# Optimization experiments

Measured on AMD Instinct MI355X. Metric: run time of the kernel, lower is better.

## Reference

```python
import jax, jax.numpy as jnp
import numpy as np

STRIDE, K, PAD = 2, 4, 1
DN = ('NCH', 'OIH', 'NCH')


def conv1d(x, w, b):
    # w: (out, in, k); stride-2, pad-1 conv matching nn.Conv1d(k=4,s=2,p=1)
    y = jax.lax.conv_general_dilated(x, w, (STRIDE,), ((PAD, PAD),), dimension_numbers=DN)
    return y + b[None, :, None]


def conv_transpose1d(x, w, b):
    # w: (in, out, k) torch ConvTranspose1d layout. Equivalent forward conv:
    # dilate input by stride, pad k-1-p=2 each side, flipped+transposed kernel.
    wf = jnp.flip(w, -1).transpose(1, 0, 2)  # (out, in, k)
    y = jax.lax.conv_general_dilated(x, wf, (1,), ((K - 1 - PAD, K - 1 - PAD),),
                                     lhs_dilation=(STRIDE,), dimension_numbers=DN)
    return y + b[None, :, None]


def setup_inputs() -> dict:
    key = jax.random.key(0)
    ks = jax.random.split(key, 9)
    s = 0.1  # keep activations stable through 6 layers
    return {
        'x': jax.random.normal(ks[0], (16, 1, 65536), dtype=jnp.float32),
        'enc_w0': jax.random.normal(ks[1], (64, 1, 4), dtype=jnp.float32) * s,
        'enc_w': jax.random.normal(ks[2], (5, 64, 64, 4), dtype=jnp.float32) * s,
        'enc_b': jax.random.normal(ks[3], (6, 64), dtype=jnp.float32) * s,
        'codebook': jax.random.normal(ks[4], (1024, 64), dtype=jnp.float32),
        'dec_w': jax.random.normal(ks[5], (5, 64, 64, 4), dtype=jnp.float32) * s,
        'dec_w_last': jax.random.normal(ks[6], (64, 1, 4), dtype=jnp.float32) * s,
        'dec_b': jax.random.normal(ks[7], (5, 64), dtype=jnp.float32) * s,
        'dec_b_last': jax.random.normal(ks[8], (1,), dtype=jnp.float32) * s,
    }


def reference(x, enc_w0, enc_w, enc_b, codebook, dec_w, dec_w_last, dec_b, dec_b_last):
    B = x.shape[0]
    D = codebook.shape[1]

    h = jax.nn.relu(conv1d(x, enc_w0, enc_b[0]))
    for i in range(5):
        h = jax.nn.relu(conv1d(h, enc_w[i], enc_b[i + 1]))
    # h: (B, D, L'); flatten tokens
    z_e = h.transpose(0, 2, 1).reshape(-1, D)  # (B*L', D)

    # ---- Vector quantize: squared-distance argmin + gather ----
    dist = (jnp.sum(z_e * z_e, axis=1, keepdims=True)
            - 2.0 * z_e @ codebook.T
            + jnp.sum(codebook * codebook, axis=1)[None, :])  # (B*L', C)
    ids = jnp.argmin(dist, axis=-1)
    e = codebook[ids]
    e_k = z_e + jax.lax.stop_gradient(e - z_e)  # straight-through

    g = e_k.reshape(B, -1, D).transpose(0, 2, 1)  # (B, D, L')

    for i in range(5):
        g = jax.nn.relu(conv_transpose1d(g, dec_w[i], dec_b[i]))
    y = conv_transpose1d(g, dec_w_last, dec_b_last)
    return y, z_e, ids
```

## Files before the change

kernel.cpp:

```cpp
#include <hip/hip_runtime.h>

#define CH 64

typedef short s16x8 __attribute__((ext_vector_type(8)));
typedef float f32x4 __attribute__((ext_vector_type(4)));

static __device__ __forceinline__ ushort f2bf(float f) {
    union { float f; uint u; } v; v.f = f;
    const uint r = (v.u + 0x7FFFu + ((v.u >> 16) & 1u)) >> 16;
    return (ushort)r;
}
static __device__ __forceinline__ float bf2f(ushort u) {
    union { uint u; float f; } v; v.u = ((uint)u) << 16; return v.f;
}

__global__ __launch_bounds__(256) void k_prepack_enc(
    const float* __restrict__ enc_w, float* __restrict__ encW)
{
    const int idx = blockIdx.x * 256 + threadIdx.x;
    const int tau = idx & 3;
    const int o = (idx >> 2) & 63;
    const int i = (idx >> 8) & 63;
    const int L = idx >> 14;
    encW[idx] = enc_w[(((size_t)L * 64 + o) * 64 + i) * 4 + tau];
}

#define ACC4(A, W, L, H) \
    A = fmaf((W).w, (H).y, fmaf((W).z, (H).x, fmaf((W).y, (L).y, fmaf((W).x, (L).x, (A)))))

template<int T>
__device__ __forceinline__ void conv_accum_t(
    const float (*inT)[2 * T + 8], const float* __restrict__ wpk, int ibase,
    float acc[4][T / 16], int og, int pg)
{
    const float* wI = wpk + og * 16 + (size_t)ibase * 256;
    for (int ii = 0; ii < 16; ++ii) {
        const float* wp = wI + ii * 256;
        const float4 w0 = *(const float4*)(wp + 0);
        const float4 w1 = *(const float4*)(wp + 4);
        const float4 w2 = *(const float4*)(wp + 8);
        const float4 w3 = *(const float4*)(wp + 12);
        const float* row = inT[ii];
#pragma unroll
        for (int j = 0; j < T / 32; ++j) {
            const int base = 4 * pg + 64 * j;
            const float2 xa = *(const float2*)(row + base);
            const float2 xb = *(const float2*)(row + base + 2);
            const float2 xc = *(const float2*)(row + base + 4);
            ACC4(acc[0][2*j],   w0, xa, xb);
            ACC4(acc[1][2*j],   w1, xa, xb);
            ACC4(acc[2][2*j],   w2, xa, xb);
            ACC4(acc[3][2*j],   w3, xa, xb);
            ACC4(acc[0][2*j+1], w0, xb, xc);
            ACC4(acc[1][2*j+1], w1, xb, xc);
            ACC4(acc[2][2*j+1], w2, xb, xc);
            ACC4(acc[3][2*j+1], w3, xb, xc);
        }
    }
}

template<int T>
__device__ __forceinline__ void conv_epilogue_t(
    float acc[4][T / 16], float* __restrict__ out,
    int b, int m0, int Lout, int transpose, int og, int pg)
{
    if (!transpose) {
#pragma unroll
        for (int oo = 0; oo < 4; ++oo) {
            float* ob = out + ((size_t)b * CH + og * 4 + oo) * Lout + m0 + 2 * pg;
#pragma unroll
            for (int j = 0; j < T / 32; ++j) {
                float2 v;
                v.x = fmaxf(acc[oo][2*j], 0.f);
                v.y = fmaxf(acc[oo][2*j+1], 0.f);
                *(float2*)(ob + 32 * j) = v;
            }
        }
    } else {
#pragma unroll
        for (int j = 0; j < T / 32; ++j)
#pragma unroll
            for (int h = 0; h < 2; ++h) {
                const int ml = 2 * pg + 32 * j + h;
                float* ob = out + ((size_t)b * Lout + m0 + ml) * CH + og * 4;
                float4 v;
                v.x = fmaxf(acc[0][2*j+h], 0.f);
                v.y = fmaxf(acc[1][2*j+h], 0.f);
                v.z = fmaxf(acc[2][2*j+h], 0.f);
                v.w = fmaxf(acc[3][2*j+h], 0.f);
                *(float4*)ob = v;
            }
    }
}

template<int T>
__global__ __launch_bounds__(256) void k_enc_conv_t(
    const float* __restrict__ in, const float* __restrict__ wpk,
    const float* __restrict__ bias, float* __restrict__ out,
    int Lin, int Lout, int transpose)
{
    __shared__ float inT[16][2 * T + 8];
    const int m0 = blockIdx.x * T;
    const int b = blockIdx.y;
    const int tid = threadIdx.x;
    const int og = tid >> 4, pg = tid & 15;
    const float* inb = in + (size_t)b * CH * Lin;
    float acc[4][T / 16];
#pragma unroll
    for (int oo = 0; oo < 4; ++oo) {
        const float bv = bias[og * 4 + oo];
#pragma unroll
        for (int j = 0; j < T / 16; ++j) acc[oo][j] = bv;
    }
    for (int q = 0; q < 4; ++q) {
        {
            const int r = tid >> 4;
            const int i = q * 16 + r;
            const int seg = tid & 15;
            const float* src = inb + (size_t)i * Lin + 2 * m0 + (T / 8) * seg;
            float* dst = inT[r] + 1 + (T / 8) * seg;
#pragma unroll
            for (int t = 0; t < T / 32; ++t) {
                const float4 v = *(const float4*)(src + 4 * t);
                float* d = dst + 4 * t;
                d[0] = v.x;
                *(float2*)(d + 1) = make_float2(v.y, v.z);
                d[3] = v.w;
            }
            if (tid < 32) {
                const int rr = tid & 15, side = tid >> 4;
                const int pl = side ? (2 * T + 1) : 0;
                const int p = 2 * m0 - 1 + pl;
                inT[rr][pl] = (p >= 0 && p < Lin) ? inb[(size_t)(q * 16 + rr) * Lin + p] : 0.f;
            }
        }
        __syncthreads();
        conv_accum_t<T>(inT, wpk, q * 16, acc, og, pg);
        __syncthreads();
    }
    conv_epilogue_t<T>(acc, out, b, m0, Lout, transpose, og, pg);
}

__global__ __launch_bounds__(256) void k_enc01(
    const float* __restrict__ x, const float* __restrict__ w0,
    const float* __restrict__ b0, const float* __restrict__ wpk0,
    const float* __restrict__ b1, float* __restrict__ out)
{
    __shared__ float xl[520];
    __shared__ float e0s[16][264];
    const int m0 = blockIdx.x * 128;
    const int b = blockIdx.y;
    const int tid = threadIdx.x;
    const int og = tid >> 4, pg = tid & 15;
    const bool interior = (blockIdx.x != 0) && (blockIdx.x != gridDim.x - 1);
    const float* xb = x + (size_t)b * 65536;
    const int x0i = 4 * m0 - 3;
    if (interior) {
        for (int xi = tid; xi < 518; xi += 256) xl[xi] = xb[x0i + xi];
    } else {
        for (int xi = tid; xi < 518; xi += 256) {
            const int q = x0i + xi;
            xl[xi] = (q >= 0 && q < 65536) ? xb[q] : 0.f;
        }
    }
    float acc[4][8];
#pragma unroll
    for (int oo = 0; oo < 4; ++oo) {
        const float bv = b1[og * 4 + oo];
#pragma unroll
        for (int j = 0; j < 8; ++j) acc[oo][j] = bv;
    }
    const int r = tid >> 4;
    const int oct = tid & 15;
    const int pbase = 2 * m0 - 1;
    __syncthreads();
    for (int q = 0; q < 4; ++q) {
        {
            const int i = q * 16 + r;
            const float4 wv = *(const float4*)(w0 + i * 4);
            const float bv = b0[i];
            if (interior) {
                for (int t = 0; t < 17; ++t) {
                    const int pl = oct * 17 + t;
                    if (pl < 258) {
                        const float* xp = xl + 2 * pl;
                        const float v = fmaf(wv.w, xp[3], fmaf(wv.z, xp[2],
                                        fmaf(wv.y, xp[1], fmaf(wv.x, xp[0], bv))));
                        e0s[r][pl] = fmaxf(v, 0.f);
                    }
                }
            } else {
                for (int t = 0; t < 17; ++t) {
                    const int pl = oct * 17 + t;
                    if (pl < 258) {
                        const int pe = pbase + pl;
                        const float* xp = xl + 2 * pl;
                        const float v = fmaf(wv.w, xp[3], fmaf(wv.z, xp[2],
                                        fmaf(wv.y, xp[1], fmaf(wv.x, xp[0], bv))));
                        e0s[r][pl] = (pe >= 0 && pe < 32768) ? fmaxf(v, 0.f) : 0.f;
                    }
                }
            }
        }
        __syncthreads();
        conv_accum_t<128>(e0s, wpk0, q * 16, acc, og, pg);
        __syncthreads();
    }
    conv_epilogue_t<128>(acc, out, b, m0, 16384, 0, og, pg);
}

__global__ __launch_bounds__(512) void k_vq(
    const float* __restrict__ z, const float* __restrict__ cb,
    float* __restrict__ idsf, ushort* __restrict__ g)
{
    __shared__ float c2s[1024];
    __shared__ float rval[8][64];
    __shared__ int   ridx[8][64];
    __shared__ int   widx[64];
    const int t0 = blockIdx.x * 64;
    const int tid = threadIdx.x;
    const int lane = tid & 63;
    const int wv = __builtin_amdgcn_readfirstlane(tid >> 6);

    for (int c = tid; c < 1024; c += 512) {
        const float* cp = cb + (size_t)c * 64;
        float s0 = 0.f, s1 = 0.f, s2 = 0.f, s3 = 0.f;
#pragma unroll
        for (int d = 0; d < 64; d += 4) {
            const float4 v = *(const float4*)(cp + d);
            s0 += v.x * v.x; s1 += v.y * v.y; s2 += v.z * v.z; s3 += v.w * v.w;
        }
        c2s[c] = (s0 + s1) + (s2 + s3);
    }
    float pz[64];
    {
        const float* zp = z + (size_t)(t0 + lane) * 64;
#pragma unroll
        for (int d = 0; d < 64; d += 4) {
            const float4 v = *(const float4*)(zp + d);
            pz[d] = -2.f * v.x; pz[d + 1] = -2.f * v.y;
            pz[d + 2] = -2.f * v.z; pz[d + 3] = -2.f * v.w;
        }
    }
    __syncthreads();
    float best = 3.0e38f; int bidx = 0;
    const int cbase = wv * 128;
    for (int cc = 0; cc < 128; ++cc) {
        const int code = cbase + cc;
        const float* cp = cb + (size_t)code * 64;
        float a0 = 0.f, a1 = 0.f, a2 = 0.f, a3 = 0.f;
#pragma unroll
        for (int d = 0; d < 64; d += 4) {
            a0 += cp[d] * pz[d];
            a1 += cp[d + 1] * pz[d + 1];
            a2 += cp[d + 2] * pz[d + 2];
            a3 += cp[d + 3] * pz[d + 3];
        }
        const float dist = c2s[code] + ((a0 + a1) + (a2 + a3));
        if (dist < best) { best = dist; bidx = code; }
    }
    rval[wv][lane] = best; ridx[wv][lane] = bidx;
    __syncthreads();
    if (tid < 64) {
        float bv = rval[0][tid]; int bi = ridx[0][tid];
#pragma unroll
        for (int k2 = 1; k2 < 8; ++k2) {
            const float v = rval[k2][tid];
            if (v < bv) { bv = v; bi = ridx[k2][tid]; }
        }
        widx[tid] = bi;
        idsf[t0 + tid] = (float)bi;
    }
    __syncthreads();
    const int bb = t0 >> 10;
    const int mb = t0 & 1023;
    ushort* gb = g + ((size_t)bb * 1026 + 1 + mb) * 64;
    for (int e = tid; e < 4096; e += 512) {
        const int d = e & 63;
        const int tok = e >> 6;
        gb[(size_t)tok * 64 + d] = f2bf(cb[(size_t)widx[tok] * 64 + d]);
    }
    if (mb == 0 && tid < 16) {
        ushort4 zz = {0, 0, 0, 0};
        *(ushort4*)(g + ((size_t)bb * 1026) * 64 + tid * 4) = zz;
    }
    if (mb == 960 && tid < 16) {
        ushort4 zz = {0, 0, 0, 0};
        *(ushort4*)(g + ((size_t)bb * 1026 + 1025) * 64 + tid * 4) = zz;
    }
}

__global__ __launch_bounds__(256) void k_prepack(
    const float* __restrict__ dec_w, ushort* __restrict__ Afrag)
{
    const int idx = blockIdx.x * 256 + threadIdx.x;
    const int j    = idx & 7;
    const int lane = (idx >> 3) & 63;
    const int kt   = (idx >> 9) & 1;
    const int m    = (idx >> 10) & 3;
    const int tap  = (idx >> 12) & 3;
    const int L    = idx >> 14;
    const int o = m * 16 + (lane & 15);
    const int i = kt * 32 + ((lane >> 4) << 3) + j;
    Afrag[idx] = f2bf(dec_w[(((size_t)L * 64 + i) * 64 + o) * 4 + tap]);
}

template<int NCG>
__global__ __launch_bounds__(64) void k_dec2t(
    const ushort* __restrict__ Xt, const ushort* __restrict__ AfragL,
    const float* __restrict__ bias, ushort* __restrict__ Yt, int Lin)
{
    const int u0 = blockIdx.x * (16 * NCG);
    const int b  = blockIdx.y;
    const int tid = threadIdx.x;
    const int Lout = Lin * 2;
    const ushort* Xb = Xt + ((size_t)b * (Lin + 2) + 1) * 64;
    ushort* Yb = Yt + ((size_t)b * (Lout + 2) + 1) * 64;

    const int lane = tid & 63;
    const int col = lane & 15, kg = lane >> 4;
    s16x8 Bm1[NCG][2], B0[NCG][2], Bp1[NCG][2];
#pragma unroll
    for (int g = 0; g < NCG; ++g) {
        const ushort* basep = Xb + (size_t)(u0 + col + 16 * g) * 64 + kg * 8;
#pragma unroll
        for (int kt = 0; kt < 2; ++kt) {
            Bm1[g][kt] = *(const s16x8*)(basep - 64 + kt * 32);
            B0[g][kt]  = *(const s16x8*)(basep + kt * 32);
            Bp1[g][kt] = *(const s16x8*)(basep + 64 + kt * 32);
        }
    }
    const s16x8* Af = (const s16x8*)AfragL;
#pragma unroll
    for (int m = 0; m < 4; ++m) {
        s16x8 a1[2], a3[2], a2[2], a0[2];
#pragma unroll
        for (int kt = 0; kt < 2; ++kt) {
            a1[kt] = Af[((1 * 4 + m) * 2 + kt) * 64 + lane];
            a3[kt] = Af[((3 * 4 + m) * 2 + kt) * 64 + lane];
            a2[kt] = Af[((2 * 4 + m) * 2 + kt) * 64 + lane];
            a0[kt] = Af[((0 * 4 + m) * 2 + kt) * 64 + lane];
        }
        const float4 bm4 = *(const float4*)(bias + m * 16 + kg * 4);
        const float bb[4] = {bm4.x, bm4.y, bm4.z, bm4.w};
#pragma unroll
        for (int g = 0; g < NCG; ++g) {
            f32x4 aE = {0.f, 0.f, 0.f, 0.f};
            f32x4 aO = {0.f, 0.f, 0.f, 0.f};
#pragma unroll
            for (int kt = 0; kt < 2; ++kt) {
                aE = __builtin_amdgcn_mfma_f32_16x16x32_bf16(a1[kt], B0[g][kt],  aE, 0, 0, 0);
                aE = __builtin_amdgcn_mfma_f32_16x16x32_bf16(a3[kt], Bm1[g][kt], aE, 0, 0, 0);
                aO = __builtin_amdgcn_mfma_f32_16x16x32_bf16(a2[kt], B0[g][kt],  aO, 0, 0, 0);
                aO = __builtin_amdgcn_mfma_f32_16x16x32_bf16(a0[kt], Bp1[g][kt], aO, 0, 0, 0);
            }
            const size_t n2 = 2 * (size_t)(u0 + col + 16 * g);
            ushort4 pe, po;
            pe.x = f2bf(fmaxf(aE[0] + bb[0], 0.f));
            pe.y = f2bf(fmaxf(aE[1] + bb[1], 0.f));
            pe.z = f2bf(fmaxf(aE[2] + bb[2], 0.f));
            pe.w = f2bf(fmaxf(aE[3] + bb[3], 0.f));
            po.x = f2bf(fmaxf(aO[0] + bb[0], 0.f));
            po.y = f2bf(fmaxf(aO[1] + bb[1], 0.f));
            po.z = f2bf(fmaxf(aO[2] + bb[2], 0.f));
            po.w = f2bf(fmaxf(aO[3] + bb[3], 0.f));
            *(ushort4*)(Yb + n2 * 64 + m * 16 + kg * 4) = pe;
            *(ushort4*)(Yb + (n2 + 1) * 64 + m * 16 + kg * 4) = po;
        }
    }
    if (blockIdx.x == 0 && tid < 16) {
        ushort4 zz = {0, 0, 0, 0};
        *(ushort4*)(Yt + ((size_t)b * (Lout + 2)) * 64 + tid * 4) = zz;
    }
    if (u0 + 16 * NCG >= Lin && tid < 16) {
        ushort4 zz = {0, 0, 0, 0};
        *(ushort4*)(Yb + (size_t)Lout * 64 + tid * 4) = zz;
    }
}

__global__ __launch_bounds__(256) void k_dec4y(
    const ushort* __restrict__ Xt, const ushort* __restrict__ AfragL,
    const float* __restrict__ w4, const float* __restrict__ bias,
    const float* __restrict__ wl, const float* __restrict__ blp,
    float* __restrict__ y)
{
    __shared__ float d4s[64][130];
    const int u0 = blockIdx.x * 64;
    const int b  = blockIdx.y;
    const int tid = threadIdx.x;
    const int Lin = 16384;
    const ushort* Xb = Xt + ((size_t)b * (Lin + 2) + 1) * 64;

    const int lane = tid & 63;
    const int wave = tid >> 6;
    const int col = lane & 15, kg = lane >> 4;
    const int ul = wave * 16 + col;
    const ushort* basep = Xb + (size_t)(u0 + ul) * 64 + kg * 8;
    s16x8 Bm1[2], B0[2], Bp1[2];
#pragma unroll
    for (int kt = 0; kt < 2; ++kt) {
        Bm1[kt] = *(const s16x8*)(basep - 64 + kt * 32);
        B0[kt]  = *(const s16x8*)(basep + kt * 32);
        Bp1[kt] = *(const s16x8*)(basep + 64 + kt * 32);
    }
    const s16x8* Af = (const s16x8*)AfragL;
#pragma unroll
    for (int m = 0; m < 4; ++m) {
        f32x4 aE = {0.f, 0.f, 0.f, 0.f};
        f32x4 aO = {0.f, 0.f, 0.f, 0.f};
#pragma unroll
        for (int kt = 0; kt < 2; ++kt) {
            aE = __builtin_amdgcn_mfma_f32_16x16x32_bf16(
                Af[((1 * 4 + m) * 2 + kt) * 64 + lane], B0[kt], aE, 0, 0, 0);
            aE = __builtin_amdgcn_mfma_f32_16x16x32_bf16(
                Af[((3 * 4 + m) * 2 + kt) * 64 + lane], Bm1[kt], aE, 0, 0, 0);
            aO = __builtin_amdgcn_mfma_f32_16x16x32_bf16(
                Af[((2 * 4 + m) * 2 + kt) * 64 + lane], B0[kt], aO, 0, 0, 0);
            aO = __builtin_amdgcn_mfma_f32_16x16x32_bf16(
                Af[((0 * 4 + m) * 2 + kt) * 64 + lane], Bp1[kt], aO, 0, 0, 0);
        }
        const float4 bm4 = *(const float4*)(bias + m * 16 + kg * 4);
        const float bb[4] = {bm4.x, bm4.y, bm4.z, bm4.w};
#pragma unroll
        for (int r = 0; r < 4; ++r) {
            const int o = m * 16 + kg * 4 + r;
            d4s[o][2 * ul + 1] = fmaxf(aE[r] + bb[r], 0.f);
            d4s[o][2 * ul + 2] = fmaxf(aO[r] + bb[r], 0.f);
        }
    }
    {
        const int side = tid >> 7;
        const int o = (tid >> 1) & 63;
        const int half = tid & 1;
        const int ib = half * 32;
        float p0 = 0.f, p1 = 0.f;
        const ushort* r0 = Xb + (size_t)(side ? (u0 + 64) : (u0 - 1)) * 64;
        const ushort* r1 = Xb + (size_t)(side ? (u0 + 63) : u0) * 64;
        const int tA = side ? 1 : 2;
        const int tB = side ? 3 : 0;
        for (int i = ib; i < ib + 32; i += 2) {
            const float* wpa = w4 + ((size_t)i * 64 + o) * 4;
            const float* wpb = w4 + ((size_t)(i + 1) * 64 + o) * 4;
            p0 += wpa[tA] * bf2f(r0[i]) + wpa[tB] * bf2f(r1[i]);
            p1 += wpb[tA] * bf2f(r0[i + 1]) + wpb[tB] * bf2f(r1[i + 1]);
        }
        float part = p0 + p1;
        part += __shfl_xor(part, 1);
        if (half == 0) {
            const float acc = bias[o] + part;
            if (side == 0) d4s[o][0]   = (u0 > 0)          ? fmaxf(acc, 0.f) : 0.f;
            else           d4s[o][129] = (u0 + 64 < 16384) ? fmaxf(acc, 0.f) : 0.f;
        }
    }
    __syncthreads();
    {
        const int odd = tid & 1;
        const int vl = (tid >> 1) + 1;
        float a0 = 0.f, a1 = 0.f, a2 = 0.f, a3 = 0.f;
        for (int o = 0; o < 64; o += 4) {
            const float4 w0 = *(const float4*)(wl + (o + 0) * 4);
            const float4 w1 = *(const float4*)(wl + (o + 1) * 4);
            const float4 w2 = *(const float4*)(wl + (o + 2) * 4);
            const float4 w3 = *(const float4*)(wl + (o + 3) * 4);
            const float xv0 = d4s[o + 0][vl], xn0 = d4s[o + 0][odd ? vl + 1 : vl - 1];
            const float xv1 = d4s[o + 1][vl], xn1 = d4s[o + 1][odd ? vl + 1 : vl - 1];
            const float xv2 = d4s[o + 2][vl], xn2 = d4s[o + 2][odd ? vl + 1 : vl - 1];
            const float xv3 = d4s[o + 3][vl], xn3 = d4s[o + 3][odd ? vl + 1 : vl - 1];
            a0 += odd ? (w0.z * xv0 + w0.x * xn0) : (w0.y * xv0 + w0.w * xn0);
            a1 += odd ? (w1.z * xv1 + w1.x * xn1) : (w1.y * xv1 + w1.w * xn1);
            a2 += odd ? (w2.z * xv2 + w2.x * xn2) : (w2.y * xv2 + w2.w * xn2);
            a3 += odd ? (w3.z * xv3 + w3.x * xn3) : (w3.y * xv3 + w3.w * xn3);
        }
        y[(size_t)b * 65536 + 4 * u0 + tid] = blp[0] + ((a0 + a1) + (a2 + a3));
    }
}

extern "C" void kernel_launch(void* const* d_in, const int* in_sizes, int n_in,
                              void* d_out, int out_size, void* d_ws, size_t ws_size,
                              hipStream_t stream) {
    const float* x      = (const float*)d_in[0];
    const float* enc_w0 = (const float*)d_in[1];
    const float* enc_w  = (const float*)d_in[2];
    const float* enc_b  = (const float*)d_in[3];
    const float* cb     = (const float*)d_in[4];
    const float* dec_w  = (const float*)d_in[5];
    const float* dec_wl = (const float*)d_in[6];
    const float* dec_b  = (const float*)d_in[7];
    const float* dec_bl = (const float*)d_in[8];
    float* y    = (float*)d_out;
    float* z_e  = y + 1048576;
    float* idsf = y + 2097152;

    float* A  = (float*)d_ws;
    float* Bf = A + 16777216;

    float*  encW  = y + 14 * 65536;
    ushort* Afrag = (ushort*)(encW + 81920);

    k_prepack_enc<<<dim3(320), 256, 0, stream>>>(enc_w, encW);
    k_prepack<<<dim3(320), 256, 0, stream>>>(dec_w, Afrag);

    k_enc01<<<dim3(128, 16), 256, 0, stream>>>(x, enc_w0, enc_b, encW, enc_b + 64, A);
    k_enc_conv_t<128><<<dim3(64, 16), 256, 0, stream>>>(A,  encW + 1 * 16384, enc_b + 2 * 64, Bf, 16384, 8192, 0);
    k_enc_conv_t<64><<<dim3(64, 16),  256, 0, stream>>>(Bf, encW + 2 * 16384, enc_b + 3 * 64, A,  8192,  4096, 0);
    k_enc_conv_t<32><<<dim3(64, 16),  256, 0, stream>>>(A,  encW + 3 * 16384, enc_b + 4 * 64, Bf, 4096,  2048, 0);
    k_enc_conv_t<32><<<dim3(32, 16),  256, 0, stream>>>(Bf, encW + 4 * 16384, enc_b + 5 * 64, z_e, 2048, 1024, 1);
    k_vq<<<256, 512, 0, stream>>>(z_e, cb, idsf, (ushort*)A);

    k_dec2t<1><<<dim3(64, 16),  64, 0, stream>>>((const ushort*)A,  Afrag + 0 * 16384, dec_b + 0 * 64, (ushort*)Bf, 1024);
    k_dec2t<2><<<dim3(64, 16),  64, 0, stream>>>((const ushort*)Bf, Afrag + 1 * 16384, dec_b + 1 * 64, (ushort*)A,  2048);
    k_dec2t<2><<<dim3(128, 16), 64, 0, stream>>>((const ushort*)A,  Afrag + 2 * 16384, dec_b + 2 * 64, (ushort*)Bf, 4096);
    k_dec2t<2><<<dim3(256, 16), 64, 0, stream>>>((const ushort*)Bf, Afrag + 3 * 16384, dec_b + 3 * 64, (ushort*)A,  8192);
    (void)hipMemcpyAsync(Bf, Afrag + 4 * 16384, 16384 * sizeof(ushort),
                         hipMemcpyDeviceToDevice, stream);
    k_dec4y<<<dim3(256, 16), 256, 0, stream>>>((const ushort*)A, (const ushort*)Bf,
                                               dec_w + 4 * 16384, dec_b + 4 * 64,
                                               dec_wl, dec_bl, y);
}
```

Baseline: 495.3 us.

## Unfuse last decoder layers into MFMA layer plus separate final-projection kernel

Replaces the fused k_dec4y kernel, which recomputed halo columns with scalar FMAs and used a shared-memory tile, with two steps. First, the reused k_dec2t MFMA kernel writes an unpadded bf16 intermediate. Second, a simple k_y kernel computes the 64-to-1 transposed conv directly from that intermediate, processing the batch in two halves to bound workspace use. Separately, the encoder's global-to-shared load is changed to a lane-interleaved stride so that adjacent threads read contiguous float4s for coalescing. The cost is an extra global round trip of the layer-5 activation and two additional launches.

```diff
diff --git a/kernel.cpp b/kernel.cpp
--- a/kernel.cpp
+++ b/kernel.cpp
@@ -117,12 +117,12 @@
             const int r = tid >> 4;
             const int i = q * 16 + r;
             const int seg = tid & 15;
-            const float* src = inb + (size_t)i * Lin + 2 * m0 + (T / 8) * seg;
-            float* dst = inT[r] + 1 + (T / 8) * seg;
+            const float* src = inb + (size_t)i * Lin + 2 * m0 + 4 * seg;
+            float* dst = inT[r] + 1 + 4 * seg;
 #pragma unroll
             for (int t = 0; t < T / 32; ++t) {
-                const float4 v = *(const float4*)(src + 4 * t);
-                float* d = dst + 4 * t;
+                const float4 v = *(const float4*)(src + 64 * t);
+                float* d = dst + 64 * t;
                 d[0] = v.x;
                 *(float2*)(d + 1) = make_float2(v.y, v.z);
                 d[3] = v.w;
@@ -305,7 +305,7 @@
     Afrag[idx] = f2bf(dec_w[(((size_t)L * 64 + i) * 64 + o) * 4 + tap]);
 }
 
-template<int NCG>
+template<int NCG, bool PAD>
 __global__ __launch_bounds__(64) void k_dec2t(
     const ushort* __restrict__ Xt, const ushort* __restrict__ AfragL,
     const float* __restrict__ bias, ushort* __restrict__ Yt, int Lin)
@@ -315,7 +315,8 @@
     const int tid = threadIdx.x;
     const int Lout = Lin * 2;
     const ushort* Xb = Xt + ((size_t)b * (Lin + 2) + 1) * 64;
-    ushort* Yb = Yt + ((size_t)b * (Lout + 2) + 1) * 64;
+    ushort* Yb = PAD ? Yt + ((size_t)b * (Lout + 2) + 1) * 64
+                     : Yt + (size_t)b * Lout * 64;
 
     const int lane = tid & 63;
     const int col = lane & 15, kg = lane >> 4;
@@ -368,111 +369,51 @@
             *(ushort4*)(Yb + (n2 + 1) * 64 + m * 16 + kg * 4) = po;
         }
     }
-    if (blockIdx.x == 0 && tid < 16) {
-        ushort4 zz = {0, 0, 0, 0};
-        *(ushort4*)(Yt + ((size_t)b * (Lout + 2)) * 64 + tid * 4) = zz;
-    }
-    if (u0 + 16 * NCG >= Lin && tid < 16) {
-        ushort4 zz = {0, 0, 0, 0};
-        *(ushort4*)(Yb + (size_t)Lout * 64 + tid * 4) = zz;
-    }
-}
-
-__global__ __launch_bounds__(256) void k_dec4y(
-    const ushort* __restrict__ Xt, const ushort* __restrict__ AfragL,
-    const float* __restrict__ w4, const float* __restrict__ bias,
-    const float* __restrict__ wl, const float* __restrict__ blp,
-    float* __restrict__ y)
-{
-    __shared__ float d4s[64][130];
-    const int u0 = blockIdx.x * 64;
-    const int b  = blockIdx.y;
-    const int tid = threadIdx.x;
-    const int Lin = 16384;
-    const ushort* Xb = Xt + ((size_t)b * (Lin + 2) + 1) * 64;
-
-    const int lane = tid & 63;
-    const int wave = tid >> 6;
-    const int col = lane & 15, kg = lane >> 4;
-    const int ul = wave * 16 + col;
-    const ushort* basep = Xb + (size_t)(u0 + ul) * 64 + kg * 8;
-    s16x8 Bm1[2], B0[2], Bp1[2];
-#pragma unroll
-    for (int kt = 0; kt < 2; ++kt) {
-        Bm1[kt] = *(const s16x8*)(basep - 64 + kt * 32);
-        B0[kt]  = *(const s16x8*)(basep + kt * 32);
-        Bp1[kt] = *(const s16x8*)(basep + 64 + kt * 32);
-    }
-    const s16x8* Af = (const s16x8*)AfragL;
-#pragma unroll
-    for (int m = 0; m < 4; ++m) {
-        f32x4 aE = {0.f, 0.f, 0.f, 0.f};
-        f32x4 aO = {0.f, 0.f, 0.f, 0.f};
-#pragma unroll
-        for (int kt = 0; kt < 2; ++kt) {
-            aE = __builtin_amdgcn_mfma_f32_16x16x32_bf16(
-                Af[((1 * 4 + m) * 2 + kt) * 64 + lane], B0[kt], aE, 0, 0, 0);
-            aE = __builtin_amdgcn_mfma_f32_16x16x32_bf16(
-                Af[((3 * 4 + m) * 2 + kt) * 64 + lane], Bm1[kt], aE, 0, 0, 0);
-            aO = __builtin_amdgcn_mfma_f32_16x16x32_bf16(
-                Af[((2 * 4 + m) * 2 + kt) * 64 + lane], B0[kt], aO, 0, 0, 0);
-            aO = __builtin_amdgcn_mfma_f32_16x16x32_bf16(
-                Af[((0 * 4 + m) * 2 + kt) * 64 + lane], Bp1[kt], aO, 0, 0, 0);
-        }
-        const float4 bm4 = *(const float4*)(bias + m * 16 + kg * 4);
-        const float bb[4] = {bm4.x, bm4.y, bm4.z, bm4.w};
-#pragma unroll
-        for (int r = 0; r < 4; ++r) {
-            const int o = m * 16 + kg * 4 + r;
-            d4s[o][2 * ul + 1] = fmaxf(aE[r] + bb[r], 0.f);
-            d4s[o][2 * ul + 2] = fmaxf(aO[r] + bb[r], 0.f);
-        }
-    }
-    {
-        const int side = tid >> 7;
-        const int o = (tid >> 1) & 63;
-        const int half = tid & 1;
-        const int ib = half * 32;
-        float p0 = 0.f, p1 = 0.f;
-        const ushort* r0 = Xb + (size_t)(side ? (u0 + 64) : (u0 - 1)) * 64;
-        const ushort* r1 = Xb + (size_t)(side ? (u0 + 63) : u0) * 64;
-        const int tA = side ? 1 : 2;
-        const int tB = side ? 3 : 0;
-        for (int i = ib; i < ib + 32; i += 2) {
-            const float* wpa = w4 + ((size_t)i * 64 + o) * 4;
-            const float* wpb = w4 + ((size_t)(i + 1) * 64 + o) * 4;
-            p0 += wpa[tA] * bf2f(r0[i]) + wpa[tB] * bf2f(r1[i]);
-            p1 += wpb[tA] * bf2f(r0[i + 1]) + wpb[tB] * bf2f(r1[i + 1]);
-        }
-        float part = p0 + p1;
-        part += __shfl_xor(part, 1);
-        if (half == 0) {
-            const float acc = bias[o] + part;
-            if (side == 0) d4s[o][0]   = (u0 > 0)          ? fmaxf(acc, 0.f) : 0.f;
-            else           d4s[o][129] = (u0 + 64 < 16384) ? fmaxf(acc, 0.f) : 0.f;
-        }
-    }
-    __syncthreads();
-    {
-        const int odd = tid & 1;
-        const int vl = (tid >> 1) + 1;
-        float a0 = 0.f, a1 = 0.f, a2 = 0.f, a3 = 0.f;
-        for (int o = 0; o < 64; o += 4) {
-            const float4 w0 = *(const float4*)(wl + (o + 0) * 4);
-            const float4 w1 = *(const float4*)(wl + (o + 1) * 4);
-            const float4 w2 = *(const float4*)(wl + (o + 2) * 4);
-            const float4 w3 = *(const float4*)(wl + (o + 3) * 4);
-            const float xv0 = d4s[o + 0][vl], xn0 = d4s[o + 0][odd ? vl + 1 : vl - 1];
-            const float xv1 = d4s[o + 1][vl], xn1 = d4s[o + 1][odd ? vl + 1 : vl - 1];
-            const float xv2 = d4s[o + 2][vl], xn2 = d4s[o + 2][odd ? vl + 1 : vl - 1];
-            const float xv3 = d4s[o + 3][vl], xn3 = d4s[o + 3][odd ? vl + 1 : vl - 1];
-            a0 += odd ? (w0.z * xv0 + w0.x * xn0) : (w0.y * xv0 + w0.w * xn0);
-            a1 += odd ? (w1.z * xv1 + w1.x * xn1) : (w1.y * xv1 + w1.w * xn1);
-            a2 += odd ? (w2.z * xv2 + w2.x * xn2) : (w2.y * xv2 + w2.w * xn2);
-            a3 += odd ? (w3.z * xv3 + w3.x * xn3) : (w3.y * xv3 + w3.w * xn3);
-        }
-        y[(size_t)b * 65536 + 4 * u0 + tid] = blp[0] + ((a0 + a1) + (a2 + a3));
-    }
+    if (PAD) {
+        if (blockIdx.x == 0 && tid < 16) {
+            ushort4 zz = {0, 0, 0, 0};
+            *(ushort4*)(Yt + ((size_t)b * (Lout + 2)) * 64 + tid * 4) = zz;
+        }
+        if (u0 + 16 * NCG >= Lin && tid < 16) {
+            ushort4 zz = {0, 0, 0, 0};
+            *(ushort4*)(Yb + (size_t)Lout * 64 + tid * 4) = zz;
+        }
+    }
+}
+
+__global__ __launch_bounds__(256) void k_y(
+    const ushort* __restrict__ d4t, const float* __restrict__ wl,
+    const float* __restrict__ blp, float* __restrict__ y, int bbase)
+{
+    const int v = blockIdx.x * 256 + threadIdx.x;
+    const int b = blockIdx.y;
+    const ushort* r0 = d4t + ((size_t)b * 32768 + v) * 64;
+    const bool hm = v > 0, hp = v < 32767;
+    const ushort* rm = hm ? r0 - 64 : r0;
+    const ushort* rp = hp ? r0 + 64 : r0;
+    const s16x8 zv = {0, 0, 0, 0, 0, 0, 0, 0};
+    float y0a = 0.f, y0b = 0.f, y1a = 0.f, y1b = 0.f;
+#pragma unroll
+    for (int c = 0; c < 8; ++c) {
+        const s16x8 a0 = *(const s16x8*)(r0 + 8 * c);
+        s16x8 am = *(const s16x8*)(rm + 8 * c);
+        s16x8 ap = *(const s16x8*)(rp + 8 * c);
+        if (!hm) am = zv;
+        if (!hp) ap = zv;
+#pragma unroll
+        for (int e = 0; e < 8; e += 2) {
+            const float4 wA = *(const float4*)(wl + (8 * c + e) * 4);
+            const float4 wB = *(const float4*)(wl + (8 * c + e + 1) * 4);
+            y0a = fmaf(wA.y, bf2f((ushort)a0[e]),     fmaf(wA.w, bf2f((ushort)am[e]),     y0a));
+            y1a = fmaf(wA.z, bf2f((ushort)a0[e]),     fmaf(wA.x, bf2f((ushort)ap[e]),     y1a));
+            y0b = fmaf(wB.y, bf2f((ushort)a0[e + 1]), fmaf(wB.w, bf2f((ushort)am[e + 1]), y0b));
+            y1b = fmaf(wB.z, bf2f((ushort)a0[e + 1]), fmaf(wB.x, bf2f((ushort)ap[e + 1]), y1b));
+        }
+    }
+    float2 out;
+    out.x = blp[0] + (y0a + y0b);
+    out.y = blp[0] + (y1a + y1b);
+    *(float2*)(y + (size_t)(bbase + b) * 65536 + 2 * v) = out;
 }
 
 extern "C" void kernel_launch(void* const* d_in, const int* in_sizes, int n_in,
@@ -507,13 +448,15 @@
     k_enc_conv_t<32><<<dim3(32, 16),  256, 0, stream>>>(Bf, encW + 4 * 16384, enc_b + 5 * 64, z_e, 2048, 1024, 1);
     k_vq<<<256, 512, 0, stream>>>(z_e, cb, idsf, (ushort*)A);
 
-    k_dec2t<1><<<dim3(64, 16),  64, 0, stream>>>((const ushort*)A,  Afrag + 0 * 16384, dec_b + 0 * 64, (ushort*)Bf, 1024);
-    k_dec2t<2><<<dim3(64, 16),  64, 0, stream>>>((const ushort*)Bf, Afrag + 1 * 16384, dec_b + 1 * 64, (ushort*)A,  2048);
-    k_dec2t<2><<<dim3(128, 16), 64, 0, stream>>>((const ushort*)A,  Afrag + 2 * 16384, dec_b + 2 * 64, (ushort*)Bf, 4096);
-    k_dec2t<2><<<dim3(256, 16), 64, 0, stream>>>((const ushort*)Bf, Afrag + 3 * 16384, dec_b + 3 * 64, (ushort*)A,  8192);
-    (void)hipMemcpyAsync(Bf, Afrag + 4 * 16384, 16384 * sizeof(ushort),
-                         hipMemcpyDeviceToDevice, stream);
-    k_dec4y<<<dim3(256, 16), 256, 0, stream>>>((const ushort*)A, (const ushort*)Bf,
-                                               dec_w + 4 * 16384, dec_b + 4 * 64,
-                                               dec_wl, dec_bl, y);
-}
+    k_dec2t<1, true><<<dim3(64, 16),  64, 0, stream>>>((const ushort*)A,  Afrag + 0 * 16384, dec_b + 0 * 64, (ushort*)Bf, 1024);
+    k_dec2t<2, true><<<dim3(64, 16),  64, 0, stream>>>((const ushort*)Bf, Afrag + 1 * 16384, dec_b + 1 * 64, (ushort*)A,  2048);
+    k_dec2t<2, true><<<dim3(128, 16), 64, 0, stream>>>((const ushort*)A,  Afrag + 2 * 16384, dec_b + 2 * 64, (ushort*)Bf, 4096);
+    k_dec2t<2, true><<<dim3(256, 16), 64, 0, stream>>>((const ushort*)Bf, Afrag + 3 * 16384, dec_b + 3 * 64, (ushort*)A,  8192);
+
+    for (int q = 0; q < 2; ++q) {
+        k_dec2t<2, false><<<dim3(512, 8), 64, 0, stream>>>(
+            (const ushort*)A + (size_t)(q * 8) * 16386 * 64,
+            Afrag + 4 * 16384, dec_b + 4 * 64, (ushort*)Bf, 16384);
+        k_y<<<dim3(128, 8), 256, 0, stream>>>((const ushort*)Bf, dec_wl, dec_bl, y, q * 8);
+    }
+}
```

Measured after the change: 455.5 us. -8.0%, faster.
